# Kernel optimization log

Hardware: AMD Instinct MI355X
Metric: run time of the kernel (lower is better)

Reference implementation:

```python
import jax, jax.numpy as jnp
import numpy as np

B, DM, DR, DE, E, H, EPS = 4096, 1024, 2048, 1024, 8, 8, 1e-5
SCALE = (DE // H) ** -0.5


def setup_inputs() -> dict:
    key = jax.random.key(0)
    ks = jax.random.split(key, 24)
    n = lambda k, s, sc=0.02: jax.random.normal(k, s, jnp.float32) * sc
    return {
        "x": n(ks[0], (B, DM), 1.0),
        "Wm_mu": n(ks[1], (E, DM, DE)), "bm_mu": jnp.zeros((E, DE)),
        "g_mu": jnp.ones((E, DE)), "be_mu": jnp.zeros((E, DE)),
        "rm_mu": jnp.zeros((E, DE)), "rv_mu": jnp.ones((E, DE)),
        "Wm_d": n(ks[2], (E, DM, DE)), "bm_d": jnp.zeros((E, DE)),
        "g_d": jnp.ones((E, DE)), "be_d": jnp.zeros((E, DE)),
        "rm_d": jnp.zeros((E, DE)), "rv_d": jnp.ones((E, DE)),
        "gw1_mu": n(ks[3], (DM, 64)), "gb1_mu": jnp.zeros((64,)),
        "gw2_mu": n(ks[4], (64, E)), "gb2_mu": jnp.zeros((E,)),
        "gw1_d": n(ks[5], (DM, 64)), "gb1_d": jnp.zeros((64,)),
        "gw2_d": n(ks[6], (64, E)), "gb2_d": jnp.zeros((E,)),
        "Wq": n(ks[7], (DE, DE)), "Wk": n(ks[8], (DE, DE)), "Wv": n(ks[9], (DE, DE)),
        "Wp": n(ks[10], (DE, DE)), "bp": jnp.zeros((DE,)),
        "se_w1": n(ks[11], (DE, DE // 64)), "se_w2": n(ks[12], (DE // 64, DE)),
        "Wr_dec": n(ks[13], (DE, DR)), "br_dec": jnp.zeros((DR,)),
        "gr": jnp.ones((DR,)), "betar": jnp.zeros((DR,)),
        "rmr": jnp.zeros((DR,)), "rvr": jnp.ones((DR,)),
        "Wm_dec": n(ks[14], (DE, DM)), "bm_dec": jnp.zeros((DM,)),
        "gm": jnp.ones((DM,)), "betam": jnp.zeros((DM,)),
        "rmm": jnp.zeros((DM,)), "rvm": jnp.ones((DM,)),
    }


def _bn(h, g, b, rm, rv):  # eval-mode BatchNorm1d
    return (h - rm) * jax.lax.rsqrt(rv + EPS) * g + b


def _moe(x, W, bias, g, be, rm, rv, gw1, gb1, gw2, gb2, act):
    # all-expert Linear+BN+act, gated softmax mixture
    h = jnp.einsum('bd,edh->beh', x, W) + bias            # [B,E,DE]
    h = act(_bn(h, g, be, rm, rv))
    gate = jax.nn.softmax(jax.nn.relu(x @ gw1 + gb1) @ gw2 + gb2, axis=-1)  # [B,E]
    return jnp.einsum('beh,be->bh', h, gate)


def _attn(x, Wq, Wk, Wv, Wp, bp):  # x: [B,N,C], self-attention (context = x)
    b, n, c = x.shape
    hd = c // H
    q = (x @ Wq).reshape(b, n, H, hd).transpose(0, 2, 1, 3)
    k = (x @ Wk).reshape(b, n, H, hd).transpose(0, 2, 1, 3)
    v = (x @ Wv).reshape(b, n, H, hd).transpose(0, 2, 1, 3)
    a = jax.nn.softmax(jnp.einsum('bhnd,bhmd->bhnm', q, k) * SCALE, axis=-1)
    o = jnp.einsum('bhnm,bhmd->bhnd', a, v).transpose(0, 2, 1, 3).reshape(b, n, c)
    return o @ Wp + bp


def reference(x, Wm_mu, bm_mu, g_mu, be_mu, rm_mu, rv_mu,
              Wm_d, bm_d, g_d, be_d, rm_d, rv_d,
              gw1_mu, gb1_mu, gw2_mu, gb2_mu, gw1_d, gb1_d, gw2_d, gb2_d,
              Wq, Wk, Wv, Wp, bp, se_w1, se_w2,
              Wr_dec, br_dec, gr, betar, rmr, rvr,
              Wm_dec, bm_dec, gm, betam, rmm, rvm):
    # Translator.test_model(x, 'MET') == forward_with_MET(x, 'test')
    mu = _moe(x, Wm_mu, bm_mu, g_mu, be_mu, rm_mu, rv_mu,
              gw1_mu, gb1_mu, gw2_mu, gb2_mu, jax.nn.relu)
    d = _moe(x, Wm_d, bm_d, g_d, be_d, rm_d, rv_d,
             gw1_d, gb1_d, gw2_d, gb2_d, jax.nn.relu)
    attn_out = _attn(x[:, None, :], Wq, Wk, Wv, Wp, bp)[:, 0, :]
    mu = mu + attn_out
    latent = mu  # forward_type == 'test'
    # SE layer
    latent = latent * jax.nn.sigmoid(jax.nn.relu(latent @ se_w1) @ se_w2)
    r_out = jax.nn.sigmoid(_bn(latent @ Wr_dec + br_dec, gr, betar, rmr, rvr))
    m_out = jax.nn.sigmoid(_bn(latent @ Wm_dec + bm_dec, gm, betam, rmm, rvm))
    return (r_out, m_out, mu, d)
```

## Files before the change

kernel.cpp:

```cpp
#include <hip/hip_runtime.h>
#include <hip/hip_bf16.h>

typedef __hip_bfloat16 bf16;
typedef __attribute__((ext_vector_type(4))) float f32x4;
typedef __attribute__((ext_vector_type(8))) short s16x8;
typedef __attribute__((ext_vector_type(4))) short s16x4;

#define AS1 __attribute__((address_space(1)))
#define AS3 __attribute__((address_space(3)))

#define NB      4096
#define EPSV    1e-5f

#define OUT_R_OFF   0ull
#define OUT_M_OFF   8388608ull
#define OUT_MU_OFF  12582912ull
#define OUT_D_OFF   16777216ull

__device__ __forceinline__ short f2bf(float f) {
  union { bf16 b; short s; } u;
  u.b = __float2bfloat16(f);
  return u.s;
}
__device__ __forceinline__ float bf2f(short s) {
  union { float f; unsigned u; } v;
  v.u = ((unsigned)(unsigned short)s) << 16;
  return v.f;
}

__device__ __forceinline__ void gl_lds16(const bf16* g, void* l) {
  __builtin_amdgcn_global_load_lds((const AS1 unsigned int*)g,
                                   (AS3 unsigned int*)l, 16, 0, 0);
}

__device__ __forceinline__ void stage_tile_ld1024(const bf16* __restrict__ base,
                                                  int row0, int k0,
                                                  unsigned char* ldsTile,
                                                  int wave, int lane) {
  const int srow = lane >> 3;
  const int gch  = ((lane & 7) + srow) & 7;
  const bf16* g0 = base + ((size_t)(row0 + srow) << 10) + k0 + (gch << 3);
#pragma unroll
  for (int i = 0; i < 4; ++i) {
    const int q = wave * 4 + i;
    gl_lds16(g0 + ((size_t)(q * 8) << 10), ldsTile + (q << 10));
  }
}

__device__ __forceinline__ s16x8 read_frag(const unsigned char* ldsTile, int r, int g) {
  return *(const s16x8*)(ldsTile + r * 128 + (((g - r) & 7) << 4));
}

struct __align__(16) TileLds {
  unsigned char A[16384];
  unsigned char Bm[16384];
  float colScale[128];
  float colShift[128];
  float rowGate[128];
};

__device__ __forceinline__ void mfma_step(const unsigned char* lA, const unsigned char* lB,
                                          int waveM, int waveN, int quad, int l15,
                                          f32x4 acc[4][4]) {
#pragma unroll
  for (int kk = 0; kk < 2; ++kk) {
    const int g = (kk << 2) + quad;
    s16x8 a[4], b[4];
#pragma unroll
    for (int i = 0; i < 4; ++i) a[i] = read_frag(lA, waveM * 64 + i * 16 + l15, g);
#pragma unroll
    for (int j = 0; j < 4; ++j) b[j] = read_frag(lB, waveN * 64 + j * 16 + l15, g);
#pragma unroll
    for (int i = 0; i < 4; ++i)
#pragma unroll
      for (int j = 0; j < 4; ++j)
        acc[i][j] = __builtin_amdgcn_mfma_f32_16x16x32_bf16(a[i], b[j], acc[i][j], 0, 0, 0);
  }
}

__global__ __launch_bounds__(256) void cvt_f32_bf16(const float* __restrict__ src,
                                                    bf16* __restrict__ dst, int n4) {
  const int i = blockIdx.x * 256 + threadIdx.x;
  if (i >= n4) return;
  const float4 v = ((const float4*)src)[i];
  s16x4 o;
  o[0] = f2bf(v.x); o[1] = f2bf(v.y); o[2] = f2bf(v.z); o[3] = f2bf(v.w);
  *(s16x4*)((short*)dst + (size_t)i * 4) = o;
}

__global__ __launch_bounds__(256) void transpose_f32_bf16(const float* __restrict__ src,
                                                          bf16* __restrict__ dstb,
                                                          int R, int C) {
  __shared__ short t[64][68];
  short* dst = (short*)dstb;
  const int tid = threadIdx.x;
  const int c0 = blockIdx.x * 64, r0 = blockIdx.y * 64;
  src += (size_t)blockIdx.z * (size_t)R * (size_t)C;
  dst += (size_t)blockIdx.z * (size_t)R * (size_t)C;
  const int cc = (tid & 15) * 4;
  const int rr = tid >> 4;
#pragma unroll
  for (int s = 0; s < 4; ++s) {
    const int lr = s * 16 + rr;
    const float4 v = *(const float4*)(src + (size_t)(r0 + lr) * C + c0 + cc);
    s16x4 o;
    o[0] = f2bf(v.x); o[1] = f2bf(v.y); o[2] = f2bf(v.z); o[3] = f2bf(v.w);
    *(s16x4*)(&t[lr][cc]) = o;
  }
  __syncthreads();
#pragma unroll
  for (int s = 0; s < 4; ++s) {
    const int wl = s * 16 + rr;
    s16x4 o;
#pragma unroll
    for (int u = 0; u < 4; ++u) o[u] = t[cc + u][wl];
    *(s16x4*)(dst + (size_t)(c0 + wl) * R + r0 + cc) = o;
  }
}

__global__ __launch_bounds__(256) void sew_prep(const float* __restrict__ w1,
                                                bf16* __restrict__ w1T) {
  const int t = blockIdx.x * 256 + threadIdx.x;
  const int u = t >> 10, d = t & 1023;
  ((short*)w1T)[t] = f2bf(w1[d * 16 + u]);
}

__global__ __launch_bounds__(256, 2) void gemm_bt(const bf16* __restrict__ A,
                                                  const bf16* __restrict__ Bt,
                                                  bf16* __restrict__ C, int N) {
  __shared__ TileLds lds;
  const int tid = threadIdx.x, lane = tid & 63, wave = tid >> 6;
  const int waveM = wave >> 1, waveN = wave & 1;
  const int quad = lane >> 4, l15 = lane & 15;
  const int m0 = blockIdx.x * 128, n0 = blockIdx.y * 128;
  f32x4 acc[4][4] = {};
  for (int kt = 0; kt < 16; ++kt) {
    __syncthreads();
    stage_tile_ld1024(A, m0, kt << 6, lds.A, wave, lane);
    stage_tile_ld1024(Bt, n0, kt << 6, lds.Bm, wave, lane);
    __builtin_amdgcn_s_waitcnt(0);
    __syncthreads();
    mfma_step(lds.A, lds.Bm, waveM, waveN, quad, l15, acc);
  }
#pragma unroll
  for (int i = 0; i < 4; ++i)
#pragma unroll
    for (int p = 0; p < 4; ++p) {
      const int r = m0 + waveM * 64 + i * 16 + (quad << 2) + p;
#pragma unroll
      for (int j = 0; j < 4; ++j) {
        const int c = n0 + waveN * 64 + j * 16 + l15;
        ((short*)C)[(size_t)r * N + c] = f2bf(acc[i][j][p]);
      }
    }
}

__global__ __launch_bounds__(256, 2) void h_gemm(const bf16* __restrict__ xb,
                                                 const bf16* __restrict__ Bg,
                                                 const float* __restrict__ gb1_mu,
                                                 const float* __restrict__ gb1_d,
                                                 float* __restrict__ H) {
  __shared__ TileLds lds;
  const int tid = threadIdx.x, lane = tid & 63, wave = tid >> 6;
  const int waveM = wave >> 1, waveN = wave & 1;
  const int quad = lane >> 4, l15 = lane & 15;
  const int m0 = blockIdx.x * 128;
  f32x4 acc[4][4] = {};
  for (int kt = 0; kt < 16; ++kt) {
    __syncthreads();
    stage_tile_ld1024(xb, m0, kt << 6, lds.A, wave, lane);
    stage_tile_ld1024(Bg, 0, kt << 6, lds.Bm, wave, lane);
    __builtin_amdgcn_s_waitcnt(0);
    __syncthreads();
    mfma_step(lds.A, lds.Bm, waveM, waveN, quad, l15, acc);
  }
  float bias[4];
#pragma unroll
  for (int j = 0; j < 4; ++j) {
    const int c = waveN * 64 + j * 16 + l15;
    bias[j] = (c < 64) ? gb1_mu[c] : gb1_d[c - 64];
  }
#pragma unroll
  for (int i = 0; i < 4; ++i)
#pragma unroll
    for (int p = 0; p < 4; ++p) {
      const int r = m0 + waveM * 64 + i * 16 + (quad << 2) + p;
#pragma unroll
      for (int j = 0; j < 4; ++j) {
        const int c = waveN * 64 + j * 16 + l15;
        H[(size_t)r * 128 + c] = fmaxf(acc[i][j][p] + bias[j], 0.f);
      }
    }
}

__global__ __launch_bounds__(256) void gates2(const float* __restrict__ H,
                                              const float* __restrict__ gw2_mu,
                                              const float* __restrict__ gb2_mu,
                                              const float* __restrict__ gw2_d,
                                              const float* __restrict__ gb2_d,
                                              float* __restrict__ gates_mu,
                                              float* __restrict__ gates_d) {
  __shared__ float w2l[1024];
  __shared__ float b2l[16];
  __shared__ float Hl[2048];
  __shared__ float lg[16][2][8];
  const int tid = threadIdx.x;
#pragma unroll
  for (int i = 0; i < 4; ++i) {
    const int idx = tid + i * 256;
    w2l[idx] = (idx < 512) ? gw2_mu[idx] : gw2_d[idx - 512];
  }
  if (tid < 16) b2l[tid] = (tid < 8) ? gb2_mu[tid] : gb2_d[tid - 8];
  const int r0 = blockIdx.x * 16;
#pragma unroll
  for (int i = 0; i < 8; ++i) {
    const int idx = tid + i * 256;
    Hl[idx] = H[(size_t)r0 * 128 + idx];
  }
  __syncthreads();
  {
    const int row = tid >> 4, pe = tid & 15, path = pe >> 3, e = pe & 7;
    float s = b2l[path * 8 + e];
    const float* hr = &Hl[row * 128 + path * 64];
    const float* wp = &w2l[path * 512];
    for (int j = 0; j < 64; ++j) s += hr[j] * wp[j * 8 + e];
    lg[row][path][e] = s;
  }
  __syncthreads();
  if (tid < 32) {
    const int row = tid >> 1, path = tid & 1;
    float mx = lg[row][path][0];
#pragma unroll
    for (int e = 1; e < 8; ++e) mx = fmaxf(mx, lg[row][path][e]);
    float ex[8], s = 0.f;
#pragma unroll
    for (int e = 0; e < 8; ++e) { ex[e] = __expf(lg[row][path][e] - mx); s += ex[e]; }
    float* gout = path ? gates_d : gates_mu;
    const float inv = 1.f / s;
#pragma unroll
    for (int e = 0; e < 8; ++e) gout[((size_t)(r0 + row) << 3) + e] = ex[e] * inv;
  }
}

__global__ __launch_bounds__(256, 2) void moe_fused(
    const bf16* __restrict__ xb, const bf16* __restrict__ WmT_mu, const bf16* __restrict__ WmT_d,
    const bf16* __restrict__ WvpT,
    const float* __restrict__ bm_mu, const float* __restrict__ g_mu, const float* __restrict__ be_mu,
    const float* __restrict__ rm_mu, const float* __restrict__ rv_mu,
    const float* __restrict__ bm_d, const float* __restrict__ g_d, const float* __restrict__ be_d,
    const float* __restrict__ rm_d, const float* __restrict__ rv_d,
    const float* __restrict__ bp,
    const float* __restrict__ gates_mu, const float* __restrict__ gates_d,
    float* __restrict__ out_mu, float* __restrict__ out_d) {
  __shared__ TileLds lds;
  const int tid = threadIdx.x, lane = tid & 63, wave = tid >> 6;
  const int waveM = wave >> 1, waveN = wave & 1;
  const int quad = lane >> 4, l15 = lane & 15;
  const int m0 = blockIdx.x * 128, n0 = blockIdx.y * 128;
  const int path = blockIdx.z;
  const int nExp = (path == 0) ? 9 : 8;
  const bf16* Wall = (path == 0) ? WmT_mu : WmT_d;
  const float* gates = (path == 0) ? gates_mu : gates_d;
  const float* bmP = (path == 0) ? bm_mu : bm_d;
  const float* gP  = (path == 0) ? g_mu : g_d;
  const float* beP = (path == 0) ? be_mu : be_d;
  const float* rmP = (path == 0) ? rm_mu : rm_d;
  const float* rvP = (path == 0) ? rv_mu : rv_d;

  f32x4 fin[4][4] = {};

  for (int e = 0; e < nExp; ++e) {
    const bool isAttn = (path == 0) && (e == 8);
    const bf16* Bmat = isAttn ? WvpT : (Wall + ((size_t)e << 20));
    f32x4 acc[4][4] = {};
    for (int kt = 0; kt < 16; ++kt) {
      __syncthreads();
      stage_tile_ld1024(xb, m0, kt << 6, lds.A, wave, lane);
      stage_tile_ld1024(Bmat, n0, kt << 6, lds.Bm, wave, lane);
      if (kt == 0 && tid < 128) {
        const int c = n0 + tid;
        float sc, sh, gt;
        if (isAttn) {
          sc = 1.f; sh = bp[c]; gt = 1.f;
        } else {
          const int idx = (e << 10) + c;
          sc = gP[idx] * rsqrtf(rvP[idx] + EPSV);
          sh = (bmP[idx] - rmP[idx]) * sc + beP[idx];
          gt = gates[((size_t)(m0 + tid) << 3) + e];
        }
        lds.colScale[tid] = sc;
        lds.colShift[tid] = sh;
        lds.rowGate[tid]  = gt;
      }
      __builtin_amdgcn_s_waitcnt(0);
      __syncthreads();
      mfma_step(lds.A, lds.Bm, waveM, waveN, quad, l15, acc);
    }
#pragma unroll
    for (int i = 0; i < 4; ++i) {
      const int rb = waveM * 64 + i * 16 + (quad << 2);
      float gt[4];
#pragma unroll
      for (int p = 0; p < 4; ++p) gt[p] = lds.rowGate[rb + p];
#pragma unroll
      for (int j = 0; j < 4; ++j) {
        const int c = waveN * 64 + j * 16 + l15;
        const float sc = lds.colScale[c], sh = lds.colShift[c];
#pragma unroll
        for (int p = 0; p < 4; ++p) {
          float v = acc[i][j][p] * sc + sh;
          if (!isAttn) v = fmaxf(v, 0.f);
          fin[i][j][p] += gt[p] * v;
        }
      }
    }
  }
  float* outp = (path == 0) ? out_mu : out_d;
#pragma unroll
  for (int i = 0; i < 4; ++i)
#pragma unroll
    for (int p = 0; p < 4; ++p) {
      const int r = m0 + waveM * 64 + i * 16 + (quad << 2) + p;
#pragma unroll
      for (int j = 0; j < 4; ++j) {
        const int c = n0 + waveN * 64 + j * 16 + l15;
        outp[((size_t)r << 10) + c] = fin[i][j][p];
      }
    }
}

__global__ __launch_bounds__(256) void se2_kernel(const float* __restrict__ mu,
                                                  const bf16* __restrict__ sw1T,
                                                  const bf16* __restrict__ sw2b,
                                                  bf16* __restrict__ latent) {
  __shared__ short w1l[16384];
  __shared__ short w2l[16384];
  __shared__ float part[4096];
  __shared__ float part2[256];
  __shared__ float s1[16];
  const int tid = threadIdx.x;
#pragma unroll
  for (int i = 0; i < 8; ++i) {
    const int idx = tid + i * 256;
    ((s16x8*)w1l)[idx] = ((const s16x8*)sw1T)[idx];
    ((s16x8*)w2l)[idx] = ((const s16x8*)sw2b)[idx];
  }
  __syncthreads();
  for (int r = 0; r < 16; ++r) {
    const int row = blockIdx.x * 16 + r;
    const float4 m = *(const float4*)(mu + ((size_t)row << 10) + tid * 4);
#pragma unroll
    for (int u = 0; u < 16; ++u) {
      const s16x4 w = *(const s16x4*)(w1l + u * 1024 + tid * 4);
      part[u * 256 + tid] = m.x * bf2f(w[0]) + m.y * bf2f(w[1])
                          + m.z * bf2f(w[2]) + m.w * bf2f(w[3]);
    }
    __syncthreads();
    {
      const int u = tid >> 4, c = tid & 15;
      float s = 0.f;
#pragma unroll
      for (int k = 0; k < 16; ++k) s += part[u * 256 + c * 16 + k];
      part2[u * 16 + c] = s;
    }
    __syncthreads();
    if (tid < 16) {
      float s = 0.f;
#pragma unroll
      for (int k = 0; k < 16; ++k) s += part2[tid * 16 + k];
      s1[tid] = fmaxf(s, 0.f);
    }
    __syncthreads();
    float o[4] = {0.f, 0.f, 0.f, 0.f};
#pragma unroll
    for (int u = 0; u < 16; ++u) {
      const s16x4 w = *(const s16x4*)(w2l + u * 1024 + tid * 4);
      const float sv = s1[u];
      o[0] += sv * bf2f(w[0]); o[1] += sv * bf2f(w[1]);
      o[2] += sv * bf2f(w[2]); o[3] += sv * bf2f(w[3]);
    }
    const float mv[4] = {m.x, m.y, m.z, m.w};
    s16x4 ov;
#pragma unroll
    for (int t = 0; t < 4; ++t)
      ov[t] = f2bf(mv[t] / (1.f + __expf(-o[t])));
    *(s16x4*)((short*)latent + ((size_t)row << 10) + tid * 4) = ov;
    __syncthreads();
  }
}

__global__ __launch_bounds__(256, 2) void dec_kernel(
    const bf16* __restrict__ latent, const bf16* __restrict__ WrT, const bf16* __restrict__ WmdT,
    const float* __restrict__ br, const float* __restrict__ gr, const float* __restrict__ betar,
    const float* __restrict__ rmr, const float* __restrict__ rvr,
    const float* __restrict__ bm, const float* __restrict__ gm, const float* __restrict__ betam,
    const float* __restrict__ rmm, const float* __restrict__ rvm,
    float* __restrict__ out) {
  __shared__ TileLds lds;
  const int tid = threadIdx.x, lane = tid & 63, wave = tid >> 6;
  const int waveM = wave >> 1, waveN = wave & 1;
  const int quad = lane >> 4, l15 = lane & 15;
  const int m0 = blockIdx.x * 128;
  const int nt = blockIdx.y;
  const bool isR = nt < 16;
  const int n0 = (isR ? nt : nt - 16) * 128;
  const bf16* Bt = isR ? WrT : WmdT;
  f32x4 acc[4][4] = {};
  for (int kt = 0; kt < 16; ++kt) {
    __syncthreads();
    stage_tile_ld1024(latent, m0, kt << 6, lds.A, wave, lane);
    stage_tile_ld1024(Bt, n0, kt << 6, lds.Bm, wave, lane);
    if (kt == 0 && tid < 128) {
      const int c = n0 + tid;
      const float bb = isR ? br[c] : bm[c];
      const float gg = isR ? gr[c] : gm[c];
      const float be = isR ? betar[c] : betam[c];
      const float rm = isR ? rmr[c] : rmm[c];
      const float rv = isR ? rvr[c] : rvm[c];
      const float sc = gg * rsqrtf(rv + EPSV);
      lds.colScale[tid] = sc;
      lds.colShift[tid] = (bb - rm) * sc + be;
    }
    __builtin_amdgcn_s_waitcnt(0);
    __syncthreads();
    mfma_step(lds.A, lds.Bm, waveM, waveN, quad, l15, acc);
  }
#pragma unroll
  for (int i = 0; i < 4; ++i)
#pragma unroll
    for (int p = 0; p < 4; ++p) {
      const int r = m0 + waveM * 64 + i * 16 + (quad << 2) + p;
#pragma unroll
      for (int j = 0; j < 4; ++j) {
        const int cl = waveN * 64 + j * 16 + l15;
        float v = acc[i][j][p] * lds.colScale[cl] + lds.colShift[cl];
        v = 1.f / (1.f + __expf(-v));
        const size_t idx = isR ? ((size_t)r * 2048 + n0 + cl)
                               : (OUT_M_OFF + (size_t)r * 1024 + n0 + cl);
        out[idx] = v;
      }
    }
}

extern "C" void kernel_launch(void* const* d_in, const int* in_sizes, int n_in,
                              void* d_out, int out_size, void* d_ws, size_t ws_size,
                              hipStream_t stream) {
  (void)in_sizes; (void)n_in; (void)out_size; (void)ws_size;
  const float* x      = (const float*)d_in[0];
  const float* Wm_mu  = (const float*)d_in[1];
  const float* bm_mu  = (const float*)d_in[2];
  const float* g_mu   = (const float*)d_in[3];
  const float* be_mu  = (const float*)d_in[4];
  const float* rm_mu  = (const float*)d_in[5];
  const float* rv_mu  = (const float*)d_in[6];
  const float* Wm_d   = (const float*)d_in[7];
  const float* bm_d   = (const float*)d_in[8];
  const float* g_d    = (const float*)d_in[9];
  const float* be_d   = (const float*)d_in[10];
  const float* rm_d   = (const float*)d_in[11];
  const float* rv_d   = (const float*)d_in[12];
  const float* gw1_mu = (const float*)d_in[13];
  const float* gb1_mu = (const float*)d_in[14];
  const float* gw2_mu = (const float*)d_in[15];
  const float* gb2_mu = (const float*)d_in[16];
  const float* gw1_d  = (const float*)d_in[17];
  const float* gb1_d  = (const float*)d_in[18];
  const float* gw2_d  = (const float*)d_in[19];
  const float* gb2_d  = (const float*)d_in[20];
  const float* Wv     = (const float*)d_in[23];
  const float* Wp     = (const float*)d_in[24];
  const float* bp     = (const float*)d_in[25];
  const float* se_w1  = (const float*)d_in[26];
  const float* se_w2  = (const float*)d_in[27];
  const float* Wr_dec = (const float*)d_in[28];
  const float* br_dec = (const float*)d_in[29];
  const float* gr     = (const float*)d_in[30];
  const float* betar  = (const float*)d_in[31];
  const float* rmr    = (const float*)d_in[32];
  const float* rvr    = (const float*)d_in[33];
  const float* Wm_dec = (const float*)d_in[34];
  const float* bm_dec = (const float*)d_in[35];
  const float* gm     = (const float*)d_in[36];
  const float* betam  = (const float*)d_in[37];
  const float* rmm    = (const float*)d_in[38];
  const float* rvm    = (const float*)d_in[39];

  unsigned char* ws = (unsigned char*)d_ws;
  bf16* xb      = (bf16*)(ws + 0);
  bf16* WmT_mu  = (bf16*)(ws + 8388608);
  bf16* WmT_d   = (bf16*)(ws + 25165824);
  bf16* WpT     = (bf16*)(ws + 25165824);
  bf16* Wv_b    = (bf16*)(ws + 27262976);
  bf16* WvpT    = (bf16*)(ws + 41943040);
  float* gates_mu = (float*)(ws + 44040192);
  float* gates_d  = (float*)(ws + 44171264);
  bf16* latent  = (bf16*)(ws + 0);
  bf16* WrT     = (bf16*)(ws + 8388608);
  bf16* WmdT    = (bf16*)(ws + 12582912);

  float* out = (float*)d_out;
  float* out_mu = out + OUT_MU_OFF;
  float* out_d  = out + OUT_D_OFF;
  float* Hb   = out + 0;
  bf16* Bg    = (bf16*)(out + 524288);
  bf16* sw1T  = (bf16*)(out + 589824);
  bf16* sw2b  = (bf16*)(out + 598016);

  const dim3 blk(256, 1, 1);

  transpose_f32_bf16<<<dim3(16, 16, 1), blk, 0, stream>>>(Wp, WpT, 1024, 1024);
  cvt_f32_bf16<<<dim3(1024, 1, 1), blk, 0, stream>>>(Wv, Wv_b, 262144);
  gemm_bt<<<dim3(8, 8, 1), blk, 0, stream>>>(WpT, Wv_b, WvpT, 1024);
  cvt_f32_bf16<<<dim3(4096, 1, 1), blk, 0, stream>>>(x, xb, 1048576);
  transpose_f32_bf16<<<dim3(1, 16, 1), blk, 0, stream>>>(gw1_mu, Bg, 1024, 64);
  transpose_f32_bf16<<<dim3(1, 16, 1), blk, 0, stream>>>(gw1_d, Bg + 65536, 1024, 64);
  h_gemm<<<dim3(32, 1, 1), blk, 0, stream>>>(xb, Bg, gb1_mu, gb1_d, Hb);
  gates2<<<dim3(256, 1, 1), blk, 0, stream>>>(Hb, gw2_mu, gb2_mu, gw2_d, gb2_d,
                                              gates_mu, gates_d);
  sew_prep<<<dim3(64, 1, 1), blk, 0, stream>>>(se_w1, sw1T);
  cvt_f32_bf16<<<dim3(16, 1, 1), blk, 0, stream>>>(se_w2, sw2b, 4096);
  transpose_f32_bf16<<<dim3(16, 16, 8), blk, 0, stream>>>(Wm_mu, WmT_mu, 1024, 1024);
  transpose_f32_bf16<<<dim3(16, 16, 8), blk, 0, stream>>>(Wm_d, WmT_d, 1024, 1024);
  moe_fused<<<dim3(32, 8, 2), blk, 0, stream>>>(
      xb, WmT_mu, WmT_d, WvpT, bm_mu, g_mu, be_mu, rm_mu, rv_mu,
      bm_d, g_d, be_d, rm_d, rv_d, bp, gates_mu, gates_d, out_mu, out_d);
  se2_kernel<<<dim3(256, 1, 1), blk, 0, stream>>>(out_mu, sw1T, sw2b, latent);
  transpose_f32_bf16<<<dim3(32, 16, 1), blk, 0, stream>>>(Wr_dec, WrT, 1024, 2048);
  transpose_f32_bf16<<<dim3(16, 16, 1), blk, 0, stream>>>(Wm_dec, WmdT, 1024, 1024);
  dec_kernel<<<dim3(32, 24, 1), blk, 0, stream>>>(
      latent, WrT, WmdT, br_dec, gr, betar, rmr, rvr,
      bm_dec, gm, betam, rmm, rvm, out);
}
```

Before: 507.2 us.

## Merge prep kernels, fuse gate GEMM with softmax, slim SE kernel

```diff
diff --git a/kernel.cpp b/kernel.cpp
--- a/kernel.cpp
+++ b/kernel.cpp
@@ -78,25 +78,10 @@
   }
 }
 
-__global__ __launch_bounds__(256) void cvt_f32_bf16(const float* __restrict__ src,
-                                                    bf16* __restrict__ dst, int n4) {
-  const int i = blockIdx.x * 256 + threadIdx.x;
-  if (i >= n4) return;
-  const float4 v = ((const float4*)src)[i];
-  s16x4 o;
-  o[0] = f2bf(v.x); o[1] = f2bf(v.y); o[2] = f2bf(v.z); o[3] = f2bf(v.w);
-  *(s16x4*)((short*)dst + (size_t)i * 4) = o;
-}
-
-__global__ __launch_bounds__(256) void transpose_f32_bf16(const float* __restrict__ src,
-                                                          bf16* __restrict__ dstb,
-                                                          int R, int C) {
-  __shared__ short t[64][68];
-  short* dst = (short*)dstb;
-  const int tid = threadIdx.x;
-  const int c0 = blockIdx.x * 64, r0 = blockIdx.y * 64;
-  src += (size_t)blockIdx.z * (size_t)R * (size_t)C;
-  dst += (size_t)blockIdx.z * (size_t)R * (size_t)C;
+__device__ __forceinline__ void tr_tile(const float* __restrict__ src,
+                                        short* __restrict__ dst,
+                                        int R, int C, int r0, int c0,
+                                        short (*t)[68], int tid) {
   const int cc = (tid & 15) * 4;
   const int rr = tid >> 4;
 #pragma unroll
@@ -118,11 +103,69 @@
   }
 }
 
-__global__ __launch_bounds__(256) void sew_prep(const float* __restrict__ w1,
-                                                bf16* __restrict__ w1T) {
-  const int t = blockIdx.x * 256 + threadIdx.x;
-  const int u = t >> 10, d = t & 1023;
-  ((short*)w1T)[t] = f2bf(w1[d * 16 + u]);
+__global__ __launch_bounds__(256) void prep_tr(
+    const float* __restrict__ Wm_mu, const float* __restrict__ Wm_d,
+    const float* __restrict__ Wp, const float* __restrict__ gw1_mu,
+    const float* __restrict__ gw1_d, const float* __restrict__ se_w1,
+    bf16* __restrict__ WmT_mu, bf16* __restrict__ WmT_d,
+    bf16* __restrict__ WpT, bf16* __restrict__ Bg, bf16* __restrict__ sw1T) {
+  __shared__ short t[64][68];
+  const int b = blockIdx.x, tid = threadIdx.x;
+  if (b < 2048) {
+    const int batch = b >> 8, rem = b & 255;
+    const size_t ofs = (size_t)batch << 20;
+    tr_tile(Wm_mu + ofs, (short*)WmT_mu + ofs, 1024, 1024,
+            (rem >> 4) * 64, (rem & 15) * 64, t, tid);
+  } else if (b < 4096) {
+    const int bb = b - 2048;
+    const int batch = bb >> 8, rem = bb & 255;
+    const size_t ofs = (size_t)batch << 20;
+    tr_tile(Wm_d + ofs, (short*)WmT_d + ofs, 1024, 1024,
+            (rem >> 4) * 64, (rem & 15) * 64, t, tid);
+  } else if (b < 4352) {
+    const int bb = b - 4096;
+    tr_tile(Wp, (short*)WpT, 1024, 1024, (bb >> 4) * 64, (bb & 15) * 64, t, tid);
+  } else if (b < 4368) {
+    tr_tile(gw1_mu, (short*)Bg, 1024, 64, (b - 4352) * 64, 0, t, tid);
+  } else if (b < 4384) {
+    tr_tile(gw1_d, (short*)Bg + 65536, 1024, 64, (b - 4368) * 64, 0, t, tid);
+  } else {
+    const int i = (b - 4384) * 256 + tid;
+    const int u = i >> 10, d = i & 1023;
+    ((short*)sw1T)[i] = f2bf(se_w1[d * 16 + u]);
+  }
+}
+
+__global__ __launch_bounds__(256) void prep_cvt(const float* __restrict__ x,
+                                                const float* __restrict__ Wv,
+                                                const float* __restrict__ se_w2,
+                                                bf16* __restrict__ xb,
+                                                bf16* __restrict__ Wv_b,
+                                                bf16* __restrict__ sw2b) {
+  const int i = blockIdx.x * 256 + threadIdx.x;
+  const float* src; bf16* dst; int idx;
+  if (i < 1048576)      { src = x;     dst = xb;   idx = i; }
+  else if (i < 1310720) { src = Wv;    dst = Wv_b; idx = i - 1048576; }
+  else if (i < 1311744) { src = se_w2; dst = sw2b; idx = i - 1310720; }
+  else return;
+  const float4 v = ((const float4*)src)[idx];
+  s16x4 o;
+  o[0] = f2bf(v.x); o[1] = f2bf(v.y); o[2] = f2bf(v.z); o[3] = f2bf(v.w);
+  *(s16x4*)((short*)dst + (size_t)idx * 4) = o;
+}
+
+__global__ __launch_bounds__(256) void prep_tr2(const float* __restrict__ Wr_dec,
+                                                const float* __restrict__ Wm_dec,
+                                                bf16* __restrict__ WrT,
+                                                bf16* __restrict__ WmdT) {
+  __shared__ short t[64][68];
+  const int b = blockIdx.x, tid = threadIdx.x;
+  if (b < 512) {
+    tr_tile(Wr_dec, (short*)WrT, 1024, 2048, (b >> 5) * 64, (b & 31) * 64, t, tid);
+  } else {
+    const int bb = b - 512;
+    tr_tile(Wm_dec, (short*)WmdT, 1024, 1024, (bb >> 4) * 64, (bb & 15) * 64, t, tid);
+  }
 }
 
 __global__ __launch_bounds__(256, 2) void gemm_bt(const bf16* __restrict__ A,
@@ -155,91 +198,77 @@
     }
 }
 
-__global__ __launch_bounds__(256, 2) void h_gemm(const bf16* __restrict__ xb,
-                                                 const bf16* __restrict__ Bg,
-                                                 const float* __restrict__ gb1_mu,
-                                                 const float* __restrict__ gb1_d,
-                                                 float* __restrict__ H) {
-  __shared__ TileLds lds;
-  const int tid = threadIdx.x, lane = tid & 63, wave = tid >> 6;
-  const int waveM = wave >> 1, waveN = wave & 1;
-  const int quad = lane >> 4, l15 = lane & 15;
-  const int m0 = blockIdx.x * 128;
-  f32x4 acc[4][4] = {};
-  for (int kt = 0; kt < 16; ++kt) {
-    __syncthreads();
-    stage_tile_ld1024(xb, m0, kt << 6, lds.A, wave, lane);
-    stage_tile_ld1024(Bg, 0, kt << 6, lds.Bm, wave, lane);
-    __builtin_amdgcn_s_waitcnt(0);
-    __syncthreads();
-    mfma_step(lds.A, lds.Bm, waveM, waveN, quad, l15, acc);
-  }
-  float bias[4];
-#pragma unroll
-  for (int j = 0; j < 4; ++j) {
-    const int c = waveN * 64 + j * 16 + l15;
-    bias[j] = (c < 64) ? gb1_mu[c] : gb1_d[c - 64];
-  }
-#pragma unroll
-  for (int i = 0; i < 4; ++i)
-#pragma unroll
-    for (int p = 0; p < 4; ++p) {
-      const int r = m0 + waveM * 64 + i * 16 + (quad << 2) + p;
-#pragma unroll
-      for (int j = 0; j < 4; ++j) {
-        const int c = waveN * 64 + j * 16 + l15;
-        H[(size_t)r * 128 + c] = fmaxf(acc[i][j][p] + bias[j], 0.f);
-      }
-    }
-}
-
-__global__ __launch_bounds__(256) void gates2(const float* __restrict__ H,
+__global__ __launch_bounds__(256) void hgates(const bf16* __restrict__ xb,
+                                              const bf16* __restrict__ Bg,
+                                              const float* __restrict__ gb1_mu,
+                                              const float* __restrict__ gb1_d,
                                               const float* __restrict__ gw2_mu,
                                               const float* __restrict__ gb2_mu,
                                               const float* __restrict__ gw2_d,
                                               const float* __restrict__ gb2_d,
                                               float* __restrict__ gates_mu,
                                               float* __restrict__ gates_d) {
+  __shared__ TileLds lds;
+  __shared__ float H[128][132];
   __shared__ float w2l[1024];
   __shared__ float b2l[16];
-  __shared__ float Hl[2048];
-  __shared__ float lg[16][2][8];
-  const int tid = threadIdx.x;
+  const int tid = threadIdx.x, lane = tid & 63, wave = tid >> 6;
+  const int waveM = wave >> 1, waveN = wave & 1;
+  const int quad = lane >> 4, l15 = lane & 15;
+  const int m0 = blockIdx.x * 128;
 #pragma unroll
   for (int i = 0; i < 4; ++i) {
     const int idx = tid + i * 256;
     w2l[idx] = (idx < 512) ? gw2_mu[idx] : gw2_d[idx - 512];
   }
   if (tid < 16) b2l[tid] = (tid < 8) ? gb2_mu[tid] : gb2_d[tid - 8];
-  const int r0 = blockIdx.x * 16;
-#pragma unroll
-  for (int i = 0; i < 8; ++i) {
-    const int idx = tid + i * 256;
-    Hl[idx] = H[(size_t)r0 * 128 + idx];
-  }
+  f32x4 acc[4][4] = {};
+  for (int kt = 0; kt < 16; ++kt) {
+    __syncthreads();
+    stage_tile_ld1024(xb, m0, kt << 6, lds.A, wave, lane);
+    stage_tile_ld1024(Bg, 0, kt << 6, lds.Bm, wave, lane);
+    __builtin_amdgcn_s_waitcnt(0);
+    __syncthreads();
+    mfma_step(lds.A, lds.Bm, waveM, waveN, quad, l15, acc);
+  }
+  float bias[4];
+#pragma unroll
+  for (int j = 0; j < 4; ++j) {
+    const int c = waveN * 64 + j * 16 + l15;
+    bias[j] = (c < 64) ? gb1_mu[c] : gb1_d[c - 64];
+  }
+#pragma unroll
+  for (int i = 0; i < 4; ++i)
+#pragma unroll
+    for (int p = 0; p < 4; ++p) {
+      const int r = waveM * 64 + i * 16 + (quad << 2) + p;
+#pragma unroll
+      for (int j = 0; j < 4; ++j) {
+        const int c = waveN * 64 + j * 16 + l15;
+        H[r][c] = fmaxf(acc[i][j][p] + bias[j], 0.f);
+      }
+    }
   __syncthreads();
-  {
-    const int row = tid >> 4, pe = tid & 15, path = pe >> 3, e = pe & 7;
-    float s = b2l[path * 8 + e];
-    const float* hr = &Hl[row * 128 + path * 64];
-    const float* wp = &w2l[path * 512];
-    for (int j = 0; j < 64; ++j) s += hr[j] * wp[j * 8 + e];
-    lg[row][path][e] = s;
-  }
-  __syncthreads();
-  if (tid < 32) {
-    const int row = tid >> 1, path = tid & 1;
-    float mx = lg[row][path][0];
-#pragma unroll
-    for (int e = 1; e < 8; ++e) mx = fmaxf(mx, lg[row][path][e]);
-    float ex[8], s = 0.f;
-#pragma unroll
-    for (int e = 0; e < 8; ++e) { ex[e] = __expf(lg[row][path][e] - mx); s += ex[e]; }
-    float* gout = path ? gates_d : gates_mu;
-    const float inv = 1.f / s;
-#pragma unroll
-    for (int e = 0; e < 8; ++e) gout[((size_t)(r0 + row) << 3) + e] = ex[e] * inv;
-  }
+  const int row = tid >> 1, path = tid & 1;
+  float lg[8];
+#pragma unroll
+  for (int e = 0; e < 8; ++e) lg[e] = b2l[path * 8 + e];
+  const float* wp = &w2l[path * 512];
+  for (int j = 0; j < 64; ++j) {
+    const float hv = H[row][path * 64 + j];
+#pragma unroll
+    for (int e = 0; e < 8; ++e) lg[e] += hv * wp[j * 8 + e];
+  }
+  float mx = lg[0];
+#pragma unroll
+  for (int e = 1; e < 8; ++e) mx = fmaxf(mx, lg[e]);
+  float s = 0.f;
+#pragma unroll
+  for (int e = 0; e < 8; ++e) { lg[e] = __expf(lg[e] - mx); s += lg[e]; }
+  const float inv = 1.f / s;
+  float* gout = path ? gates_d : gates_mu;
+#pragma unroll
+  for (int e = 0; e < 8; ++e) gout[((size_t)(m0 + row) << 3) + e] = lg[e] * inv;
 }
 
 __global__ __launch_bounds__(256, 2) void moe_fused(
@@ -329,52 +358,43 @@
     }
 }
 
-__global__ __launch_bounds__(256) void se2_kernel(const float* __restrict__ mu,
+__global__ __launch_bounds__(256) void se3_kernel(const float* __restrict__ mu,
                                                   const bf16* __restrict__ sw1T,
                                                   const bf16* __restrict__ sw2b,
                                                   bf16* __restrict__ latent) {
-  __shared__ short w1l[16384];
-  __shared__ short w2l[16384];
-  __shared__ float part[4096];
-  __shared__ float part2[256];
+  __shared__ float part[16][256];
+  __shared__ float part2[16][17];
   __shared__ float s1[16];
   const int tid = threadIdx.x;
-#pragma unroll
-  for (int i = 0; i < 8; ++i) {
-    const int idx = tid + i * 256;
-    ((s16x8*)w1l)[idx] = ((const s16x8*)sw1T)[idx];
-    ((s16x8*)w2l)[idx] = ((const s16x8*)sw2b)[idx];
-  }
-  __syncthreads();
-  for (int r = 0; r < 16; ++r) {
-    const int row = blockIdx.x * 16 + r;
+  for (int r = 0; r < 8; ++r) {
+    const int row = blockIdx.x * 8 + r;
     const float4 m = *(const float4*)(mu + ((size_t)row << 10) + tid * 4);
 #pragma unroll
     for (int u = 0; u < 16; ++u) {
-      const s16x4 w = *(const s16x4*)(w1l + u * 1024 + tid * 4);
-      part[u * 256 + tid] = m.x * bf2f(w[0]) + m.y * bf2f(w[1])
-                          + m.z * bf2f(w[2]) + m.w * bf2f(w[3]);
+      const s16x4 w = *(const s16x4*)((const short*)sw1T + u * 1024 + tid * 4);
+      part[u][tid] = m.x * bf2f(w[0]) + m.y * bf2f(w[1])
+                   + m.z * bf2f(w[2]) + m.w * bf2f(w[3]);
     }
     __syncthreads();
     {
       const int u = tid >> 4, c = tid & 15;
       float s = 0.f;
 #pragma unroll
-      for (int k = 0; k < 16; ++k) s += part[u * 256 + c * 16 + k];
-      part2[u * 16 + c] = s;
+      for (int k = 0; k < 16; ++k) s += part[u][c * 16 + k];
+      part2[u][c] = s;
     }
     __syncthreads();
     if (tid < 16) {
       float s = 0.f;
 #pragma unroll
-      for (int k = 0; k < 16; ++k) s += part2[tid * 16 + k];
+      for (int k = 0; k < 16; ++k) s += part2[tid][k];
       s1[tid] = fmaxf(s, 0.f);
     }
     __syncthreads();
     float o[4] = {0.f, 0.f, 0.f, 0.f};
 #pragma unroll
     for (int u = 0; u < 16; ++u) {
-      const s16x4 w = *(const s16x4*)(w2l + u * 1024 + tid * 4);
+      const s16x4 w = *(const s16x4*)((const short*)sw2b + u * 1024 + tid * 4);
       const float sv = s1[u];
       o[0] += sv * bf2f(w[0]); o[1] += sv * bf2f(w[1]);
       o[2] += sv * bf2f(w[2]); o[3] += sv * bf2f(w[3]);
@@ -489,8 +509,6 @@
   bf16* xb      = (bf16*)(ws + 0);
   bf16* WmT_mu  = (bf16*)(ws + 8388608);
   bf16* WmT_d   = (bf16*)(ws + 25165824);
-  bf16* WpT     = (bf16*)(ws + 25165824);
-  bf16* Wv_b    = (bf16*)(ws + 27262976);
   bf16* WvpT    = (bf16*)(ws + 41943040);
   float* gates_mu = (float*)(ws + 44040192);
   float* gates_d  = (float*)(ws + 44171264);
@@ -501,32 +519,27 @@
   float* out = (float*)d_out;
   float* out_mu = out + OUT_MU_OFF;
   float* out_d  = out + OUT_D_OFF;
-  float* Hb   = out + 0;
   bf16* Bg    = (bf16*)(out + 524288);
   bf16* sw1T  = (bf16*)(out + 589824);
   bf16* sw2b  = (bf16*)(out + 598016);
+  bf16* WpT   = (bf16*)(out + OUT_MU_OFF);
+  bf16* Wv_b  = (bf16*)(out + OUT_MU_OFF + 524288);
 
   const dim3 blk(256, 1, 1);
 
-  transpose_f32_bf16<<<dim3(16, 16, 1), blk, 0, stream>>>(Wp, WpT, 1024, 1024);
-  cvt_f32_bf16<<<dim3(1024, 1, 1), blk, 0, stream>>>(Wv, Wv_b, 262144);
+  prep_tr<<<dim3(4448, 1, 1), blk, 0, stream>>>(
+      Wm_mu, Wm_d, Wp, gw1_mu, gw1_d, se_w1,
+      WmT_mu, WmT_d, WpT, Bg, sw1T);
+  prep_cvt<<<dim3(5127, 1, 1), blk, 0, stream>>>(x, Wv, se_w2, xb, Wv_b, sw2b);
   gemm_bt<<<dim3(8, 8, 1), blk, 0, stream>>>(WpT, Wv_b, WvpT, 1024);
-  cvt_f32_bf16<<<dim3(4096, 1, 1), blk, 0, stream>>>(x, xb, 1048576);
-  transpose_f32_bf16<<<dim3(1, 16, 1), blk, 0, stream>>>(gw1_mu, Bg, 1024, 64);
-  transpose_f32_bf16<<<dim3(1, 16, 1), blk, 0, stream>>>(gw1_d, Bg + 65536, 1024, 64);
-  h_gemm<<<dim3(32, 1, 1), blk, 0, stream>>>(xb, Bg, gb1_mu, gb1_d, Hb);
-  gates2<<<dim3(256, 1, 1), blk, 0, stream>>>(Hb, gw2_mu, gb2_mu, gw2_d, gb2_d,
-                                              gates_mu, gates_d);
-  sew_prep<<<dim3(64, 1, 1), blk, 0, stream>>>(se_w1, sw1T);
-  cvt_f32_bf16<<<dim3(16, 1, 1), blk, 0, stream>>>(se_w2, sw2b, 4096);
-  transpose_f32_bf16<<<dim3(16, 16, 8), blk, 0, stream>>>(Wm_mu, WmT_mu, 1024, 1024);
-  transpose_f32_bf16<<<dim3(16, 16, 8), blk, 0, stream>>>(Wm_d, WmT_d, 1024, 1024);
+  hgates<<<dim3(32, 1, 1), blk, 0, stream>>>(xb, Bg, gb1_mu, gb1_d,
+                                             gw2_mu, gb2_mu, gw2_d, gb2_d,
+                                             gates_mu, gates_d);
   moe_fused<<<dim3(32, 8, 2), blk, 0, stream>>>(
       xb, WmT_mu, WmT_d, WvpT, bm_mu, g_mu, be_mu, rm_mu, rv_mu,
       bm_d, g_d, be_d, rm_d, rv_d, bp, gates_mu, gates_d, out_mu, out_d);
-  se2_kernel<<<dim3(256, 1, 1), blk, 0, stream>>>(out_mu, sw1T, sw2b, latent);
-  transpose_f32_bf16<<<dim3(32, 16, 1), blk, 0, stream>>>(Wr_dec, WrT, 1024, 2048);
-  transpose_f32_bf16<<<dim3(16, 16, 1), blk, 0, stream>>>(Wm_dec, WmdT, 1024, 1024);
+  prep_tr2<<<dim3(768, 1, 1), blk, 0, stream>>>(Wr_dec, Wm_dec, WrT, WmdT);
+  se3_kernel<<<dim3(512, 1, 1), blk, 0, stream>>>(out_mu, sw1T, sw2b, latent);
   dec_kernel<<<dim3(32, 24, 1), blk, 0, stream>>>(
       latent, WrT, WmdT, br_dec, gr, betar, rmr, rvr,
       bm_dec, gm, betam, rmm, rvm, out);
```

Measured after the change: 486.5 us. 1.04x faster.
